# Performance work log

Measured on AMD Instinct MI355X. Metric: run time of the kernel, lower is better.

## Reference

```python
import jax, jax.numpy as jnp
import numpy as np

N_USERS = 200000   # num_users (dataset.n_users)
N_EDGES = 3200000  # nnz of normalized social adjacency D^-1/2 A D^-1/2
LATENT_DIM = 64    # config['latent_dim_rec']
N_LAYERS = 3       # config['layer']


def setup_inputs() -> dict:
    key = jax.random.key(0)
    k1, k2, k3, k4 = jax.random.split(key, 4)
    return {
        "user_emb": jax.random.normal(k1, (N_USERS, LATENT_DIM), dtype=jnp.float32) * 0.1,
        "edge_vals": jax.random.uniform(k2, (N_EDGES,), dtype=jnp.float32),
        "edge_src": jax.random.randint(k3, (N_EDGES,), 0, N_USERS, dtype=jnp.int32),
        "edge_dst": jax.random.randint(k4, (N_EDGES,), 0, N_USERS, dtype=jnp.int32),
    }


def _spmm(edge_vals, edge_src, edge_dst, x):
    # out[i] = sum_{e: dst[e]==i} vals[e] * x[src[e]]  ==  torch.sparse.mm(G, x)
    msgs = edge_vals[:, None] * x[edge_src]            # [E, D]
    return jax.ops.segment_sum(msgs, edge_dst, num_segments=N_USERS)


def reference(user_emb, edge_vals, edge_src, edge_dst):
    # LightGCN.computer(): repeated SpMM propagation, then mean over layer embeddings
    h = user_emb
    acc = user_emb  # running sum instead of stack+mean (same math)
    for _ in range(N_LAYERS):
        h = _spmm(edge_vals, edge_src, edge_dst, h)
        acc = acc + h
    return acc / jnp.float32(N_LAYERS + 1)
```

## Files before the change

kernel.cpp:

```cpp
#include <hip/hip_runtime.h>


#define DIM 64
#define BUCKET_SHIFT 7
#define BUCKET_USERS 128
#define NBLK_P 256
#define SCHUNK 12544
#define MAXB 2048
typedef unsigned short u16;

__device__ inline u16 f2bf(float f) {
    unsigned u = __float_as_uint(f);
    u += 0x7fffu + ((u >> 16) & 1u);
    return (u16)(u >> 16);
}
__device__ inline float bf2f(u16 h) { return __uint_as_float(((unsigned)h) << 16); }

__global__ void conv_bf16(const float4* __restrict__ in, ushort4* __restrict__ out, int n4) {
    int i = blockIdx.x * blockDim.x + threadIdx.x;
    int stride = gridDim.x * blockDim.x;
    for (; i < n4; i += stride) {
        float4 v = in[i];
        ushort4 o;
        o.x = f2bf(v.x); o.y = f2bf(v.y); o.z = f2bf(v.z); o.w = f2bf(v.w);
        out[i] = o;
    }
}

__global__ __launch_bounds__(512)
void hist2d(const int* __restrict__ dst, int* __restrict__ cnt2d, int n_edges, int NB) {
    __shared__ int c[MAXB];
    int blk = blockIdx.x, t = threadIdx.x;
    int CH = (n_edges + NBLK_P - 1) / NBLK_P;
    int c0 = blk * CH, c1 = min(c0 + CH, n_edges);
    for (int i = t; i < NB; i += 512) c[i] = 0;
    __syncthreads();
    for (int i = c0 + t; i < c1; i += 512) atomicAdd(&c[dst[i] >> BUCKET_SHIFT], 1);
    __syncthreads();
    for (int i = t; i < NB; i += 512) cnt2d[i * NBLK_P + blk] = c[i];
}

__global__ void runstarts(const int* __restrict__ cnt2d, int* __restrict__ runst2d,
                          int* __restrict__ total, int NB) {
    int wid = (blockIdx.x * blockDim.x + threadIdx.x) >> 6;
    int lane = threadIdx.x & 63;
    if (wid >= NB) return;
    int carry = 0;
    for (int k = 0; k < NBLK_P; k += 64) {
        int cv = cnt2d[wid * NBLK_P + k + lane];
        int s = cv;
        for (int off = 1; off < 64; off <<= 1) {
            int v = __shfl_up(s, off, 64);
            if (lane >= off) s += v;
        }
        runst2d[wid * NBLK_P + k + lane] = carry + s - cv;
        carry += __shfl(s, 63, 64);
    }
    if (lane == 0) total[wid] = carry;
}

__global__ void scan_base(const int* __restrict__ cnt, int* __restrict__ base, int n) {
    __shared__ int sh[1024];
    int t = threadIdx.x;
    int C = (n + 1023) >> 10;
    int lo = t * C;
    int sum = 0;
    for (int j = 0; j < C; j++) { int idx = lo + j; if (idx < n) sum += cnt[idx]; }
    sh[t] = sum;
    __syncthreads();
    for (int off = 1; off < 1024; off <<= 1) {
        int v = (t >= off) ? sh[t - off] : 0;
        __syncthreads();
        sh[t] += v;
        __syncthreads();
    }
    int run = (t == 0) ? 0 : sh[t - 1];
    for (int j = 0; j < C; j++) {
        int idx = lo + j;
        if (idx < n) { base[idx] = run; run += cnt[idx]; }
    }
    if (t == 1023) base[n] = sh[1023];
}

__global__ __launch_bounds__(512)
void scatter_runs(const float* __restrict__ vals, const int* __restrict__ src,
                  const int* __restrict__ dst, const int* __restrict__ base,
                  const int* __restrict__ runst2d, int2* __restrict__ bins,
                  int NB, int n_edges) {
    __shared__ int2 stage[SCHUNK];
    __shared__ u16 sbk[SCHUNK];
    __shared__ int s_start[MAXB];
    __shared__ int s_cur[MAXB];
    __shared__ int s_gb[MAXB];
    __shared__ int s_tmp[512];
    int blk = blockIdx.x, t = threadIdx.x;
    int CH = (n_edges + NBLK_P - 1) / NBLK_P;
    int c0 = blk * CH, c1 = min(c0 + CH, n_edges);

    for (int i = t; i < NB; i += 512) s_start[i] = 0;
    __syncthreads();
    for (int i = c0 + t; i < c1; i += 512) atomicAdd(&s_start[dst[i] >> BUCKET_SHIFT], 1);
    __syncthreads();

    const int NPT = MAXB / 512;
    int lo = t * NPT, run = 0, loc[NPT];
#pragma unroll
    for (int j = 0; j < NPT; j++) {
        int idx = lo + j;
        int cv = (idx < NB) ? s_start[idx] : 0;
        loc[j] = run; run += cv;
    }
    s_tmp[t] = run;
    __syncthreads();
    for (int off = 1; off < 512; off <<= 1) {
        int v = (t >= off) ? s_tmp[t - off] : 0;
        __syncthreads();
        s_tmp[t] += v;
        __syncthreads();
    }
    int excl = (t == 0) ? 0 : s_tmp[t - 1];
    int totloc = s_tmp[511];
#pragma unroll
    for (int j = 0; j < NPT; j++) {
        int idx = lo + j;
        if (idx < NB) { int st = excl + loc[j]; s_start[idx] = st; s_cur[idx] = st; }
    }
    for (int i = t; i < NB; i += 512) s_gb[i] = base[i] + runst2d[i * NBLK_P + blk];
    __syncthreads();

    for (int i = c0 + t; i < c1; i += 512) {
        int d = dst[i];
        int b = d >> BUCKET_SHIFT;
        int p = atomicAdd(&s_cur[b], 1);
        stage[p] = make_int2(src[i] | ((d & (BUCKET_USERS - 1)) << 20),
                             __float_as_int(vals[i]));
        sbk[p] = (u16)b;
    }
    __syncthreads();

    for (int i = t; i < totloc; i += 512) {
        int b = sbk[i];
        bins[s_gb[b] + (i - s_start[b])] = stage[i];
    }
}

__global__ __launch_bounds__(256)
void bucket_csr(const int2* __restrict__ bins, const int* __restrict__ base,
                int2* __restrict__ csr, int* __restrict__ row_end, int n_users) {
    __shared__ int cnt[BUCKET_USERS];
    __shared__ int pos[BUCKET_USERS];
    int b = blockIdx.x;
    int t = threadIdx.x;
    for (int i = t; i < BUCKET_USERS; i += 256) cnt[i] = 0;
    __syncthreads();
    int s0 = base[b];
    int s1 = base[b + 1];
    for (int i = s0 + t; i < s1; i += 256)
        atomicAdd(&cnt[((unsigned)bins[i].x) >> 20], 1);
    __syncthreads();
    if (t < 64) {
        int c0 = cnt[2 * t], c1 = cnt[2 * t + 1];
        int s = c0 + c1;
        for (int off = 1; off < 64; off <<= 1) {
            int v = __shfl_up(s, off, 64);
            if (t >= off) s += v;
        }
        int excl = s - (c0 + c1);
        pos[2 * t] = excl;
        pos[2 * t + 1] = excl + c0;
        int u0 = b << BUCKET_SHIFT;
        if (u0 + 2 * t < n_users)     row_end[u0 + 2 * t]     = s0 + excl + c0;
        if (u0 + 2 * t + 1 < n_users) row_end[u0 + 2 * t + 1] = s0 + excl + c0 + c1;
    }
    __syncthreads();
    for (int i = s0 + t; i < s1; i += 256) {
        int2 ev = bins[i];
        int p = atomicAdd(&pos[((unsigned)ev.x) >> 20], 1);
        csr[s0 + p] = make_int2(ev.x & 0xFFFFF, ev.y);
    }
}

template <int MODE>
__global__ __launch_bounds__(256)
void spmm_bf(const int2* __restrict__ edges, const int* __restrict__ row_end,
             const u16* __restrict__ xb, u16* __restrict__ hb_out,
             const float* __restrict__ x0, float* __restrict__ acc, int n_rows) {
    int row = blockIdx.x * 4 + (threadIdx.x >> 6);
    if (row >= n_rows) return;
    int lane = threadIdx.x & 63;
    int g = lane >> 4;
    int sl = lane & 15;

    int start = (row == 0) ? 0 : row_end[row - 1];
    int end = row_end[row];

    float4 a = make_float4(0.f, 0.f, 0.f, 0.f);
    for (int e = start + g; e < end; e += 4) {
        int2 ev = edges[e];
        float v = __int_as_float(ev.y);
        ushort4 xv = *(const ushort4*)&xb[(size_t)(ev.x & 0xFFFFF) * DIM + sl * 4];
        a.x += v * bf2f(xv.x); a.y += v * bf2f(xv.y);
        a.z += v * bf2f(xv.z); a.w += v * bf2f(xv.w);
    }
    a.x += __shfl_xor(a.x, 16, 64); a.y += __shfl_xor(a.y, 16, 64);
    a.z += __shfl_xor(a.z, 16, 64); a.w += __shfl_xor(a.w, 16, 64);
    a.x += __shfl_xor(a.x, 32, 64); a.y += __shfl_xor(a.y, 32, 64);
    a.z += __shfl_xor(a.z, 32, 64); a.w += __shfl_xor(a.w, 32, 64);

    size_t gb = (size_t)row * DIM + sl * 4;
    if (MODE == 0) {
        if (g == 0) {
            ushort4 o; o.x = f2bf(a.x); o.y = f2bf(a.y); o.z = f2bf(a.z); o.w = f2bf(a.w);
            *(ushort4*)&hb_out[gb] = o;
        }
        if (g == 1) {
            float4 x0v = *(const float4*)&x0[gb];
            x0v.x += a.x; x0v.y += a.y; x0v.z += a.z; x0v.w += a.w;
            *(float4*)&acc[gb] = x0v;
        }
    } else if (MODE == 1) {
        if (g == 0) {
            ushort4 o; o.x = f2bf(a.x); o.y = f2bf(a.y); o.z = f2bf(a.z); o.w = f2bf(a.w);
            *(ushort4*)&hb_out[gb] = o;
        }
        if (g == 1) {
            float4 c = *(const float4*)&acc[gb];
            c.x += a.x; c.y += a.y; c.z += a.z; c.w += a.w;
            *(float4*)&acc[gb] = c;
        }
    } else {
        if (g == 0) {
            float4 c = *(const float4*)&acc[gb];
            c.x = (c.x + a.x) * 0.25f; c.y = (c.y + a.y) * 0.25f;
            c.z = (c.z + a.z) * 0.25f; c.w = (c.w + a.w) * 0.25f;
            *(float4*)&acc[gb] = c;
        }
    }
}

extern "C" void kernel_launch(void* const* d_in, const int* in_sizes, int n_in,
                              void* d_out, int out_size, void* d_ws, size_t ws_size,
                              hipStream_t stream) {
    const float* user_emb  = (const float*)d_in[0];
    const float* edge_vals = (const float*)d_in[1];
    const int*   edge_src  = (const int*)d_in[2];
    const int*   edge_dst  = (const int*)d_in[3];
    float* out = (float*)d_out;

    const int n_users = in_sizes[0] / DIM;
    const int n_edges = in_sizes[1];
    const size_t nfloats = (size_t)n_users * DIM;
    const int nbucket = (n_users + BUCKET_USERS - 1) >> BUCKET_SHIFT;

    auto align = [](size_t x) { return (x + 255) & ~(size_t)255; };
    char* ws = (char*)d_ws;
    int2* csr      = (int2*)ws;  ws += align((size_t)n_edges * sizeof(int2));
    int*  row_end  = (int*)ws;   ws += align((size_t)n_users * sizeof(int));
    u16*  xb0      = (u16*)ws;   ws += align(nfloats * sizeof(u16));
    char* overlayA = ws;         ws += align((size_t)n_edges * sizeof(int2));
    u16*  hb_a     = (u16*)overlayA;
    int2* bins     = (int2*)overlayA;
    u16*  hb_b     = (u16*)ws;   ws += align(nfloats * sizeof(u16));
    int*  cnt2d    = (int*)ws;   ws += align((size_t)nbucket * NBLK_P * sizeof(int));
    int*  runst2d  = (int*)ws;   ws += align((size_t)nbucket * NBLK_P * sizeof(int));
    int*  total    = (int*)ws;   ws += align((size_t)nbucket * sizeof(int));
    int*  base     = (int*)ws;

    conv_bf16<<<2048, 256, 0, stream>>>((const float4*)user_emb, (ushort4*)xb0,
                                        (int)(nfloats / 4));

    hist2d<<<NBLK_P, 512, 0, stream>>>(edge_dst, cnt2d, n_edges, nbucket);
    runstarts<<<(nbucket + 3) / 4, 256, 0, stream>>>(cnt2d, runst2d, total, nbucket);
    scan_base<<<1, 1024, 0, stream>>>(total, base, nbucket);
    scatter_runs<<<NBLK_P, 512, 0, stream>>>(edge_vals, edge_src, edge_dst,
                                             base, runst2d, bins, nbucket, n_edges);
    bucket_csr<<<nbucket, 256, 0, stream>>>(bins, base, csr, row_end, n_users);

    const int nblk = (n_users + 3) / 4;
    spmm_bf<0><<<nblk, 256, 0, stream>>>(csr, row_end, xb0, hb_a, user_emb, out, n_users);
    spmm_bf<1><<<nblk, 256, 0, stream>>>(csr, row_end, hb_a, hb_b, nullptr, out, n_users);
    spmm_bf<2><<<nblk, 256, 0, stream>>>(csr, row_end, hb_b, nullptr, nullptr, out, n_users);
}
```

Measured before the change: 561.1 us.

## Unroll SpMM edge loop 4x and defer layer accumulation to final pass

The edge loop in the SpMM kernel now issues four independent edge loads and four gathers before the FMAs. This gives more memory-level parallelism per lane. The fp32 accumulator is no longer read and written in every layer. The last layer sums x0 with the stored bf16 h1 and h2 and scales the result once, which cuts fp32 output traffic but makes the intermediate layer terms bf16-rounded in the final sum.

```diff
diff --git a/kernel.cpp b/kernel.cpp
--- a/kernel.cpp
+++ b/kernel.cpp
@@ -184,7 +184,8 @@
 __global__ __launch_bounds__(256)
 void spmm_bf(const int2* __restrict__ edges, const int* __restrict__ row_end,
              const u16* __restrict__ xb, u16* __restrict__ hb_out,
-             const float* __restrict__ x0, float* __restrict__ acc, int n_rows) {
+             const float* __restrict__ x0, const u16* __restrict__ h1,
+             const u16* __restrict__ h2, float* __restrict__ outp, int n_rows) {
     int row = blockIdx.x * 4 + (threadIdx.x >> 6);
     if (row >= n_rows) return;
     int lane = threadIdx.x & 63;
@@ -195,12 +196,28 @@
     int end = row_end[row];
 
     float4 a = make_float4(0.f, 0.f, 0.f, 0.f);
-    for (int e = start + g; e < end; e += 4) {
-        int2 ev = edges[e];
-        float v = __int_as_float(ev.y);
-        ushort4 xv = *(const ushort4*)&xb[(size_t)(ev.x & 0xFFFFF) * DIM + sl * 4];
-        a.x += v * bf2f(xv.x); a.y += v * bf2f(xv.y);
-        a.z += v * bf2f(xv.z); a.w += v * bf2f(xv.w);
+    for (int e = start + g; e < end; e += 16) {
+        int2 ev0 = edges[e];
+        int2 ev1 = make_int2(0, 0), ev2 = make_int2(0, 0), ev3 = make_int2(0, 0);
+        ushort4 xv1 = make_ushort4(0, 0, 0, 0), xv2 = xv1, xv3 = xv1;
+        bool g1 = (e + 4 < end), g2 = (e + 8 < end), g3 = (e + 12 < end);
+        if (g1) ev1 = edges[e + 4];
+        if (g2) ev2 = edges[e + 8];
+        if (g3) ev3 = edges[e + 12];
+        ushort4 xv0 = *(const ushort4*)&xb[(size_t)(ev0.x & 0xFFFFF) * DIM + sl * 4];
+        if (g1) xv1 = *(const ushort4*)&xb[(size_t)(ev1.x & 0xFFFFF) * DIM + sl * 4];
+        if (g2) xv2 = *(const ushort4*)&xb[(size_t)(ev2.x & 0xFFFFF) * DIM + sl * 4];
+        if (g3) xv3 = *(const ushort4*)&xb[(size_t)(ev3.x & 0xFFFFF) * DIM + sl * 4];
+        float v0 = __int_as_float(ev0.y), v1 = __int_as_float(ev1.y);
+        float v2 = __int_as_float(ev2.y), v3 = __int_as_float(ev3.y);
+        a.x += v0 * bf2f(xv0.x); a.y += v0 * bf2f(xv0.y);
+        a.z += v0 * bf2f(xv0.z); a.w += v0 * bf2f(xv0.w);
+        a.x += v1 * bf2f(xv1.x); a.y += v1 * bf2f(xv1.y);
+        a.z += v1 * bf2f(xv1.z); a.w += v1 * bf2f(xv1.w);
+        a.x += v2 * bf2f(xv2.x); a.y += v2 * bf2f(xv2.y);
+        a.z += v2 * bf2f(xv2.z); a.w += v2 * bf2f(xv2.w);
+        a.x += v3 * bf2f(xv3.x); a.y += v3 * bf2f(xv3.y);
+        a.z += v3 * bf2f(xv3.z); a.w += v3 * bf2f(xv3.w);
     }
     a.x += __shfl_xor(a.x, 16, 64); a.y += __shfl_xor(a.y, 16, 64);
     a.z += __shfl_xor(a.z, 16, 64); a.w += __shfl_xor(a.w, 16, 64);
@@ -208,32 +225,23 @@
     a.z += __shfl_xor(a.z, 32, 64); a.w += __shfl_xor(a.w, 32, 64);
 
     size_t gb = (size_t)row * DIM + sl * 4;
-    if (MODE == 0) {
+    if (MODE != 2) {
         if (g == 0) {
-            ushort4 o; o.x = f2bf(a.x); o.y = f2bf(a.y); o.z = f2bf(a.z); o.w = f2bf(a.w);
+            ushort4 o;
+            o.x = f2bf(a.x); o.y = f2bf(a.y); o.z = f2bf(a.z); o.w = f2bf(a.w);
             *(ushort4*)&hb_out[gb] = o;
-        }
-        if (g == 1) {
-            float4 x0v = *(const float4*)&x0[gb];
-            x0v.x += a.x; x0v.y += a.y; x0v.z += a.z; x0v.w += a.w;
-            *(float4*)&acc[gb] = x0v;
-        }
-    } else if (MODE == 1) {
-        if (g == 0) {
-            ushort4 o; o.x = f2bf(a.x); o.y = f2bf(a.y); o.z = f2bf(a.z); o.w = f2bf(a.w);
-            *(ushort4*)&hb_out[gb] = o;
-        }
-        if (g == 1) {
-            float4 c = *(const float4*)&acc[gb];
-            c.x += a.x; c.y += a.y; c.z += a.z; c.w += a.w;
-            *(float4*)&acc[gb] = c;
         }
     } else {
         if (g == 0) {
-            float4 c = *(const float4*)&acc[gb];
-            c.x = (c.x + a.x) * 0.25f; c.y = (c.y + a.y) * 0.25f;
-            c.z = (c.z + a.z) * 0.25f; c.w = (c.w + a.w) * 0.25f;
-            *(float4*)&acc[gb] = c;
+            float4 x0v = *(const float4*)&x0[gb];
+            ushort4 h1v = *(const ushort4*)&h1[gb];
+            ushort4 h2v = *(const ushort4*)&h2[gb];
+            float4 o;
+            o.x = (x0v.x + bf2f(h1v.x) + bf2f(h2v.x) + a.x) * 0.25f;
+            o.y = (x0v.y + bf2f(h1v.y) + bf2f(h2v.y) + a.y) * 0.25f;
+            o.z = (x0v.z + bf2f(h1v.z) + bf2f(h2v.z) + a.z) * 0.25f;
+            o.w = (x0v.w + bf2f(h1v.w) + bf2f(h2v.w) + a.w) * 0.25f;
+            *(float4*)&outp[gb] = o;
         }
     }
 }
@@ -277,7 +285,10 @@
     bucket_csr<<<nbucket, 256, 0, stream>>>(bins, base, csr, row_end, n_users);
 
     const int nblk = (n_users + 3) / 4;
-    spmm_bf<0><<<nblk, 256, 0, stream>>>(csr, row_end, xb0, hb_a, user_emb, out, n_users);
-    spmm_bf<1><<<nblk, 256, 0, stream>>>(csr, row_end, hb_a, hb_b, nullptr, out, n_users);
-    spmm_bf<2><<<nblk, 256, 0, stream>>>(csr, row_end, hb_b, nullptr, nullptr, out, n_users);
-}
+    spmm_bf<0><<<nblk, 256, 0, stream>>>(csr, row_end, xb0, hb_a,
+                                         nullptr, nullptr, nullptr, nullptr, n_users);
+    spmm_bf<1><<<nblk, 256, 0, stream>>>(csr, row_end, hb_a, hb_b,
+                                         nullptr, nullptr, nullptr, nullptr, n_users);
+    spmm_bf<2><<<nblk, 256, 0, stream>>>(csr, row_end, hb_b, nullptr,
+                                         user_emb, hb_a, hb_b, out, n_users);
+}
```

Result: faster. 514.1 us (-8.4%).
